# Kernel optimization log

Measured on AMD Instinct MI355X. Metric: run time of the kernel, lower is better.

Reference implementation:

```python
import jax, jax.numpy as jnp
import numpy as np

NUM_HEADS = 14
NUM_KV_HEADS = 2
HEAD_DIM = 64
HIDDEN = 896
ROPE_THETA = 1000000.0
NEG_INF = -1e9


def _rope_tables(seq_len, dtype=jnp.float32):
    inv_freq = 1.0 / (ROPE_THETA ** (jnp.arange(0, HEAD_DIM, 2, dtype=jnp.float32) / HEAD_DIM))
    t = jnp.arange(seq_len, dtype=jnp.float32)
    freqs = t[:, None] * inv_freq[None, :]          # [S, hd/2]
    emb = jnp.concatenate((freqs, freqs), axis=-1)  # [S, hd]
    return jnp.cos(emb).astype(dtype), jnp.sin(emb).astype(dtype)


def _rotate_half(x):
    x1, x2 = x[..., : x.shape[-1] // 2], x[..., x.shape[-1] // 2 :]
    return jnp.concatenate((-x2, x1), axis=-1)


def setup_inputs() -> dict:
    key = jax.random.key(0)
    ks = jax.random.split(key, 6)
    B, S = 2, 2048
    hidden_states = jax.random.normal(ks[0], (B, S, HIDDEN), dtype=jnp.float32)
    # additive causal mask [1, 1, S, S]
    causal = jnp.tril(jnp.ones((S, S), dtype=bool))
    attention_mask = jnp.where(causal, 0.0, NEG_INF).astype(jnp.float32)[None, None]
    sd = 1.0 / np.sqrt(HIDDEN)
    Wq = jax.random.normal(ks[1], (HIDDEN, NUM_HEADS * HEAD_DIM), dtype=jnp.float32) * sd
    bq = jnp.zeros((NUM_HEADS * HEAD_DIM,), dtype=jnp.float32)
    Wk = jax.random.normal(ks[2], (HIDDEN, NUM_KV_HEADS * HEAD_DIM), dtype=jnp.float32) * sd
    bk = jnp.zeros((NUM_KV_HEADS * HEAD_DIM,), dtype=jnp.float32)
    Wv = jax.random.normal(ks[3], (HIDDEN, NUM_KV_HEADS * HEAD_DIM), dtype=jnp.float32) * sd
    bv = jnp.zeros((NUM_KV_HEADS * HEAD_DIM,), dtype=jnp.float32)
    Wo = jax.random.normal(ks[4], (NUM_HEADS * HEAD_DIM, HIDDEN), dtype=jnp.float32) * sd
    return {
        'hidden_states': hidden_states, 'attention_mask': attention_mask,
        'Wq': Wq, 'bq': bq, 'Wk': Wk, 'bk': bk, 'Wv': Wv, 'bv': bv, 'Wo': Wo,
    }


def reference(hidden_states, attention_mask, Wq, bq, Wk, bk, Wv, bv, Wo):
    B, S, _ = hidden_states.shape
    n_groups = NUM_HEADS // NUM_KV_HEADS
    q = (hidden_states @ Wq + bq).reshape(B, S, NUM_HEADS, HEAD_DIM)
    k = (hidden_states @ Wk + bk).reshape(B, S, NUM_KV_HEADS, HEAD_DIM)
    v = (hidden_states @ Wv + bv).reshape(B, S, NUM_KV_HEADS, HEAD_DIM)

    cos, sin = _rope_tables(S, hidden_states.dtype)
    cos = cos[None, :, None, :]
    sin = sin[None, :, None, :]
    q = q * cos + _rotate_half(q) * sin
    k = k * cos + _rotate_half(k) * sin

    # GQA: repeat kv heads to match query heads
    k = jnp.repeat(k, n_groups, axis=2)  # [B, S, nH, hd]
    v = jnp.repeat(v, n_groups, axis=2)

    q = q.transpose(0, 2, 1, 3)  # [B, nH, S, hd]
    k = k.transpose(0, 2, 1, 3)
    v = v.transpose(0, 2, 1, 3)

    scores = jnp.einsum('bhqd,bhkd->bhqk', q, k) / jnp.sqrt(jnp.float32(HEAD_DIM)).astype(q.dtype)
    scores = scores + attention_mask
    attn = jax.nn.softmax(scores, axis=-1)
    out = jnp.einsum('bhqk,bhkd->bhqd', attn, v)        # [B, nH, S, hd]
    out = out.transpose(0, 2, 1, 3).reshape(B, S, -1)   # [B, S, nH*hd]
    return out @ Wo
```

## Files before the change

kernel.cpp:

```cpp
#include <hip/hip_runtime.h>
#include <hip/hip_bf16.h>
#include <math.h>

#define NH 14
#define NKV 2
#define HD 64
#define HID 896
#define SEQ 2048
#define BATCH 2
#define KT 28

typedef __attribute__((ext_vector_type(8))) short short8;
typedef __attribute__((ext_vector_type(4))) float f32x4;
typedef unsigned short ushort_t;

__device__ __forceinline__ unsigned short f2b(float f) {
    unsigned int u = __float_as_uint(f);
    unsigned int r = (u + 0x7fffu + ((u >> 16) & 1u)) >> 16;
    return (unsigned short)r;
}

__device__ __forceinline__ float exp2fast(float x) {
    return __builtin_amdgcn_exp2f(x);
}

__global__ __launch_bounds__(256) void xcast_kernel(
    const float* __restrict__ X, ushort_t* __restrict__ Xb)
{
    size_t i = ((size_t)blockIdx.x * 256 + threadIdx.x) * 8;
    float4 a = *(const float4*)(X + i);
    float4 b = *(const float4*)(X + i + 4);
    short8 o;
    o[0] = f2b(a.x); o[1] = f2b(a.y); o[2] = f2b(a.z); o[3] = f2b(a.w);
    o[4] = f2b(b.x); o[5] = f2b(b.y); o[6] = f2b(b.z); o[7] = f2b(b.w);
    *(short8*)(Xb + i) = o;
}

__global__ __launch_bounds__(256) void wtrans_kernel(
    const float* __restrict__ Wq, const float* __restrict__ Wk,
    const float* __restrict__ Wv, const float* __restrict__ Wo,
    ushort_t* __restrict__ WqkvT, ushort_t* __restrict__ WoT)
{
    __shared__ float tile[32][33];
    const int tx = threadIdx.x, ty = threadIdx.y;
    const int z = blockIdx.z;
    const float* src; ushort_t* dst; int N, rowoff;
    if      (z == 0) { src = Wq; dst = WqkvT; N = HID; rowoff = 0;    }
    else if (z == 1) { src = Wk; dst = WqkvT; N = 128; rowoff = 896;  }
    else if (z == 2) { src = Wv; dst = WqkvT; N = 128; rowoff = 1024; }
    else             { src = Wo; dst = WoT;   N = HID; rowoff = 0;    }
    const int k0 = blockIdx.x * 32;
    const int n0 = blockIdx.y * 32;
    if (n0 >= N) return;
    #pragma unroll
    for (int i = 0; i < 4; ++i)
        tile[ty * 4 + i][tx] = src[(size_t)(k0 + ty * 4 + i) * N + n0 + tx];
    __syncthreads();
    #pragma unroll
    for (int i = 0; i < 4; ++i)
        dst[(size_t)(rowoff + n0 + ty * 4 + i) * HID + k0 + tx]
            = f2b(tile[tx][ty * 4 + i]);
}

#define LDA 40
__global__ __launch_bounds__(256) void qkv_kernel(
    const ushort_t* __restrict__ Xb, const ushort_t* __restrict__ WqkvT,
    const float* __restrict__ bq, const float* __restrict__ bk,
    const float* __restrict__ bv,
    ushort_t* __restrict__ qbuf, ushort_t* __restrict__ kbuf,
    ushort_t* __restrict__ vbuf)
{
    __shared__ ushort_t Asb[2][128 * LDA];
    __shared__ ushort_t Bsb[2][64 * LDA];
    const int tid  = threadIdx.x;
    const int w    = tid >> 6;
    const int lane = tid & 63;
    const int quad = lane >> 4;
    const int l16  = lane & 15;
    const int m0 = blockIdx.x * 128;
    const int nt = blockIdx.y;
    const int nb = nt * 64;

    const int ar0 = tid >> 2;
    const int ac8 = tid & 3;
    const ushort_t* Ag0 = Xb + (size_t)(m0 + ar0) * HID + ac8 * 8;
    const ushort_t* Ag1 = Xb + (size_t)(m0 + ar0 + 64) * HID + ac8 * 8;
    const ushort_t* Bg  = WqkvT + (size_t)(nb + ar0) * HID + ac8 * 8;

    f32x4 acc[2][4];
    #pragma unroll
    for (int mf = 0; mf < 2; ++mf)
        #pragma unroll
        for (int nf = 0; nf < 4; ++nf) acc[mf][nf] = (f32x4){0.f, 0.f, 0.f, 0.f};

    short8 aReg0, aReg1, bReg;
    aReg0 = *(const short8*)(Ag0);
    aReg1 = *(const short8*)(Ag1);
    bReg  = *(const short8*)(Bg);
    *(short8*)&Asb[0][ar0 * LDA + ac8 * 8]        = aReg0;
    *(short8*)&Asb[0][(ar0 + 64) * LDA + ac8 * 8] = aReg1;
    *(short8*)&Bsb[0][ar0 * LDA + ac8 * 8]        = bReg;
    aReg0 = *(const short8*)(Ag0 + 32);
    aReg1 = *(const short8*)(Ag1 + 32);
    bReg  = *(const short8*)(Bg  + 32);

    for (int ks = 0; ks < KT; ++ks) {
        __syncthreads();
        const int cur = ks & 1;
        if (ks + 1 < KT) {
            *(short8*)&Asb[cur ^ 1][ar0 * LDA + ac8 * 8]        = aReg0;
            *(short8*)&Asb[cur ^ 1][(ar0 + 64) * LDA + ac8 * 8] = aReg1;
            *(short8*)&Bsb[cur ^ 1][ar0 * LDA + ac8 * 8]        = bReg;
        }
        if (ks + 2 < KT) {
            aReg0 = *(const short8*)(Ag0 + (ks + 2) * 32);
            aReg1 = *(const short8*)(Ag1 + (ks + 2) * 32);
            bReg  = *(const short8*)(Bg  + (ks + 2) * 32);
        }
        const ushort_t* Ab = &Asb[cur][(w * 32 + l16) * LDA + quad * 8];
        short8 a0 = *(const short8*)Ab;
        short8 a1 = *(const short8*)(Ab + 16 * LDA);
        #pragma unroll
        for (int nf = 0; nf < 4; ++nf) {
            short8 bf = *(const short8*)&Bsb[cur][(nf * 16 + l16) * LDA + quad * 8];
            acc[0][nf] = __builtin_amdgcn_mfma_f32_16x16x32_bf16(a0, bf, acc[0][nf], 0, 0, 0);
            acc[1][nf] = __builtin_amdgcn_mfma_f32_16x16x32_bf16(a1, bf, acc[1][nf], 0, 0, 0);
        }
    }

    float bcol[4];
    #pragma unroll
    for (int f = 0; f < 4; ++f) {
        int d = f * 16 + l16;
        bcol[f] = (nt < 14) ? bq[nt * 64 + d]
                : (nt < 16) ? bk[(nt - 14) * 64 + d]
                            : bv[(nt - 16) * 64 + d];
    }
    const float lnth = 13.815510558f;
    float if0 = expf(-((float)l16)        / 32.0f * lnth);
    float if1 = expf(-((float)(l16 + 16)) / 32.0f * lnth);

    #pragma unroll
    for (int mf = 0; mf < 2; ++mf)
        #pragma unroll
        for (int r = 0; r < 4; ++r) {
            int grow = m0 + w * 32 + mf * 16 + quad * 4 + r;
            int b = grow >> 11;
            int s = grow & 2047;
            float v0 = acc[mf][0][r] + bcol[0];
            float v1 = acc[mf][1][r] + bcol[1];
            float v2 = acc[mf][2][r] + bcol[2];
            float v3 = acc[mf][3][r] + bcol[3];
            if (nt < 16) {
                float s0, c0, s1, c1;
                sincosf((float)s * if0, &s0, &c0);
                sincosf((float)s * if1, &s1, &c1);
                float n0 = v0 * c0 - v2 * s0;
                float n2 = v2 * c0 + v0 * s0;
                float n1 = v1 * c1 - v3 * s1;
                float n3 = v3 * c1 + v1 * s1;
                v0 = n0; v1 = n1; v2 = n2; v3 = n3;
            }
            if (nt < 14) {
                const float qs = 0.18033688f;
                v0 *= qs; v1 *= qs; v2 *= qs; v3 *= qs;
                ushort_t* dst = qbuf + ((size_t)(b * NH + nt) * SEQ + s) * HD;
                dst[l16]      = f2b(v0);
                dst[l16 + 16] = f2b(v1);
                dst[l16 + 32] = f2b(v2);
                dst[l16 + 48] = f2b(v3);
            } else if (nt < 16) {
                ushort_t* dst = kbuf + ((size_t)(b * NKV + nt - 14) * SEQ + s) * HD;
                dst[l16]      = f2b(v0);
                dst[l16 + 16] = f2b(v1);
                dst[l16 + 32] = f2b(v2);
                dst[l16 + 48] = f2b(v3);
            } else {
                ushort_t* dst = vbuf + (size_t)(b * NKV + nt - 16) * HD * SEQ + s;
                dst[(size_t)(l16)      * SEQ] = f2b(v0);
                dst[(size_t)(l16 + 16) * SEQ] = f2b(v1);
                dst[(size_t)(l16 + 32) * SEQ] = f2b(v2);
                dst[(size_t)(l16 + 48) * SEQ] = f2b(v3);
            }
        }
}

#define LDP 76
#define SMMAX 12.0f
__global__ __launch_bounds__(256) void attn_kernel(
    const ushort_t* __restrict__ qbuf, const ushort_t* __restrict__ kbuf,
    const ushort_t* __restrict__ vbuf, ushort_t* __restrict__ abuf)
{
    __shared__ ushort_t Ks[64 * LDP];
    __shared__ ushort_t Vt[64 * LDP];
    __shared__ ushort_t Ps[4][16 * LDP];

    const int tid  = threadIdx.x;
    const int w    = tid >> 6;
    const int lane = tid & 63;
    const int quad = lane >> 4;
    const int l16  = lane & 15;
    const int qt = 31 - blockIdx.x;
    const int h  = blockIdx.y;
    const int b  = blockIdx.z;
    const int kvh = h / (NH / NKV);

    const ushort_t* kb_h = kbuf + (size_t)(b * NKV + kvh) * SEQ * HD;
    const ushort_t* vt_h = vbuf + (size_t)(b * NKV + kvh) * HD * SEQ;

    const int srow = tid >> 3;
    const int sc8  = tid & 7;
    const ushort_t* Kg0 = kb_h + (size_t)srow * HD + sc8 * 8;
    const ushort_t* Kg1 = kb_h + (size_t)(srow + 32) * HD + sc8 * 8;
    const ushort_t* Vg0 = vt_h + (size_t)srow * SEQ + sc8 * 8;
    const ushort_t* Vg1 = vt_h + (size_t)(srow + 32) * SEQ + sc8 * 8;

    const ushort_t* qrow =
        qbuf + ((size_t)((b * NH + h) * SEQ) + qt * 64 + w * 16 + l16) * HD;
    short8 qf0 = *(const short8*)(qrow + quad * 8);
    short8 qf1 = *(const short8*)(qrow + 32 + quad * 8);

    short8 onesb;
    #pragma unroll
    for (int i = 0; i < 8; ++i) onesb[i] = (short)0x3F80;

    f32x4 O[4];
    f32x4 La;
    #pragma unroll
    for (int n = 0; n < 4; ++n) O[n] = (f32x4){0.f, 0.f, 0.f, 0.f};
    La = (f32x4){0.f, 0.f, 0.f, 0.f};

    short8 kr0 = *(const short8*)(Kg0);
    short8 kr1 = *(const short8*)(Kg1);
    short8 vr0 = *(const short8*)(Vg0);
    short8 vr1 = *(const short8*)(Vg1);

    for (int kt = 0; kt <= qt; ++kt) {
        __syncthreads();
        *(short8*)&Ks[srow * LDP + sc8 * 8]        = kr0;
        *(short8*)&Ks[(srow + 32) * LDP + sc8 * 8] = kr1;
        *(short8*)&Vt[srow * LDP + sc8 * 8]        = vr0;
        *(short8*)&Vt[(srow + 32) * LDP + sc8 * 8] = vr1;
        __syncthreads();
        if (kt < qt) {
            kr0 = *(const short8*)(Kg0 + (size_t)(kt + 1) * 64 * HD);
            kr1 = *(const short8*)(Kg1 + (size_t)(kt + 1) * 64 * HD);
            vr0 = *(const short8*)(Vg0 + (kt + 1) * 64);
            vr1 = *(const short8*)(Vg1 + (kt + 1) * 64);
        }

        f32x4 S[4];
        #pragma unroll
        for (int f = 0; f < 4; ++f) {
            short8 kf0 = *(const short8*)&Ks[(f * 16 + l16) * LDP + quad * 8];
            short8 kf1 = *(const short8*)&Ks[(f * 16 + l16) * LDP + 32 + quad * 8];
            S[f] = (f32x4){0.f, 0.f, 0.f, 0.f};
            S[f] = __builtin_amdgcn_mfma_f32_16x16x32_bf16(qf0, kf0, S[f], 0, 0, 0);
            S[f] = __builtin_amdgcn_mfma_f32_16x16x32_bf16(qf1, kf1, S[f], 0, 0, 0);
        }

        if (kt == qt) {
            #pragma unroll
            for (int f = 0; f < 4; ++f)
                #pragma unroll
                for (int r = 0; r < 4; ++r)
                    if ((f * 16 + l16) > (w * 16 + quad * 4 + r))
                        S[f][r] = -1e30f;
        }
        #pragma unroll
        for (int f = 0; f < 4; ++f)
            #pragma unroll
            for (int r = 0; r < 4; ++r)
                Ps[w][(quad * 4 + r) * LDP + f * 16 + l16]
                    = f2b(exp2fast(S[f][r] - SMMAX));

        short8 pa0 = *(const short8*)&Ps[w][l16 * LDP + quad * 8];
        short8 pa1 = *(const short8*)&Ps[w][l16 * LDP + 32 + quad * 8];

        La = __builtin_amdgcn_mfma_f32_16x16x32_bf16(pa0, onesb, La, 0, 0, 0);
        La = __builtin_amdgcn_mfma_f32_16x16x32_bf16(pa1, onesb, La, 0, 0, 0);
        #pragma unroll
        for (int n = 0; n < 4; ++n) {
            short8 vf0 = *(const short8*)&Vt[(n * 16 + l16) * LDP + quad * 8];
            short8 vf1 = *(const short8*)&Vt[(n * 16 + l16) * LDP + 32 + quad * 8];
            O[n] = __builtin_amdgcn_mfma_f32_16x16x32_bf16(pa0, vf0, O[n], 0, 0, 0);
            O[n] = __builtin_amdgcn_mfma_f32_16x16x32_bf16(pa1, vf1, O[n], 0, 0, 0);
        }
    }

    float inv[4];
    #pragma unroll
    for (int r = 0; r < 4; ++r) inv[r] = 1.0f / La[r];
    #pragma unroll
    for (int n = 0; n < 4; ++n)
        #pragma unroll
        for (int r = 0; r < 4; ++r) {
            int rowg = qt * 64 + w * 16 + quad * 4 + r;
            abuf[(size_t)(b * SEQ + rowg) * HID + h * HD + n * 16 + l16]
                = f2b(O[n][r] * inv[r]);
        }
}

__global__ __launch_bounds__(256) void oproj_kernel(
    const ushort_t* __restrict__ A, const ushort_t* __restrict__ WoT,
    float* __restrict__ out)
{
    __shared__ ushort_t Asb[2][128 * LDA];
    __shared__ ushort_t Bsb[2][64 * LDA];
    const int tid  = threadIdx.x;
    const int w    = tid >> 6;
    const int lane = tid & 63;
    const int quad = lane >> 4;
    const int l16  = lane & 15;
    const int m0 = blockIdx.x * 128;
    const int n0 = blockIdx.y * 64;

    const int ar0 = tid >> 2;
    const int ac8 = tid & 3;
    const ushort_t* Ag0 = A + (size_t)(m0 + ar0) * HID + ac8 * 8;
    const ushort_t* Ag1 = A + (size_t)(m0 + ar0 + 64) * HID + ac8 * 8;
    const ushort_t* Bg  = WoT + (size_t)(n0 + ar0) * HID + ac8 * 8;

    f32x4 acc[2][4];
    #pragma unroll
    for (int mf = 0; mf < 2; ++mf)
        #pragma unroll
        for (int nf = 0; nf < 4; ++nf) acc[mf][nf] = (f32x4){0.f, 0.f, 0.f, 0.f};

    short8 aReg0, aReg1, bReg;
    aReg0 = *(const short8*)(Ag0);
    aReg1 = *(const short8*)(Ag1);
    bReg  = *(const short8*)(Bg);
    *(short8*)&Asb[0][ar0 * LDA + ac8 * 8]        = aReg0;
    *(short8*)&Asb[0][(ar0 + 64) * LDA + ac8 * 8] = aReg1;
    *(short8*)&Bsb[0][ar0 * LDA + ac8 * 8]        = bReg;
    aReg0 = *(const short8*)(Ag0 + 32);
    aReg1 = *(const short8*)(Ag1 + 32);
    bReg  = *(const short8*)(Bg  + 32);

    for (int ks = 0; ks < KT; ++ks) {
        __syncthreads();
        const int cur = ks & 1;
        if (ks + 1 < KT) {
            *(short8*)&Asb[cur ^ 1][ar0 * LDA + ac8 * 8]        = aReg0;
            *(short8*)&Asb[cur ^ 1][(ar0 + 64) * LDA + ac8 * 8] = aReg1;
            *(short8*)&Bsb[cur ^ 1][ar0 * LDA + ac8 * 8]        = bReg;
        }
        if (ks + 2 < KT) {
            aReg0 = *(const short8*)(Ag0 + (ks + 2) * 32);
            aReg1 = *(const short8*)(Ag1 + (ks + 2) * 32);
            bReg  = *(const short8*)(Bg  + (ks + 2) * 32);
        }
        const ushort_t* Ab = &Asb[cur][(w * 32 + l16) * LDA + quad * 8];
        short8 a0 = *(const short8*)Ab;
        short8 a1 = *(const short8*)(Ab + 16 * LDA);
        #pragma unroll
        for (int nf = 0; nf < 4; ++nf) {
            short8 bf = *(const short8*)&Bsb[cur][(nf * 16 + l16) * LDA + quad * 8];
            acc[0][nf] = __builtin_amdgcn_mfma_f32_16x16x32_bf16(a0, bf, acc[0][nf], 0, 0, 0);
            acc[1][nf] = __builtin_amdgcn_mfma_f32_16x16x32_bf16(a1, bf, acc[1][nf], 0, 0, 0);
        }
    }

    #pragma unroll
    for (int mf = 0; mf < 2; ++mf)
        #pragma unroll
        for (int r = 0; r < 4; ++r) {
            size_t rbase = (size_t)(m0 + w * 32 + mf * 16 + quad * 4 + r) * HID + n0;
            #pragma unroll
            for (int f = 0; f < 4; ++f)
                out[rbase + f * 16 + l16] = acc[mf][f][r];
        }
}

extern "C" void kernel_launch(void* const* d_in, const int* in_sizes, int n_in,
                              void* d_out, int out_size, void* d_ws, size_t ws_size,
                              hipStream_t stream) {
    const float* X  = (const float*)d_in[0];
    const float* Wq = (const float*)d_in[2];
    const float* bq = (const float*)d_in[3];
    const float* Wk = (const float*)d_in[4];
    const float* bk = (const float*)d_in[5];
    const float* Wv = (const float*)d_in[6];
    const float* bv = (const float*)d_in[7];
    const float* Wo = (const float*)d_in[8];
    float* out = (float*)d_out;

    ushort_t* ws    = (ushort_t*)d_ws;
    ushort_t* Xb    = ws;
    ushort_t* WqkvT = Xb    + 3670016;
    ushort_t* WoT   = WqkvT + 1032192;
    ushort_t* qbuf  = WoT   + 802816;
    ushort_t* kbuf  = qbuf  + 3670016;
    ushort_t* vbuf  = kbuf  + 524288;
    ushort_t* abufb = vbuf  + 524288;

    xcast_kernel<<<dim3(1792), 256, 0, stream>>>(X, Xb);
    wtrans_kernel<<<dim3(28, 28, 4), dim3(32, 8), 0, stream>>>(
        Wq, Wk, Wv, Wo, WqkvT, WoT);
    qkv_kernel<<<dim3(32, 18), 256, 0, stream>>>(
        Xb, WqkvT, bq, bk, bv, qbuf, kbuf, vbuf);
    attn_kernel<<<dim3(32, NH, BATCH), 256, 0, stream>>>(
        qbuf, kbuf, vbuf, abufb);
    oproj_kernel<<<dim3(32, 14), 256, 0, stream>>>(
        abufb, WoT, out);
}
```

Baseline: 199.3 us.

## Process two query tiles per attention block to reuse staged K/V tiles

Each attention block now handles 128 query rows, as two 64-row sub-tiles per wave set, instead of 64. Each K/V tile loaded into shared memory is used by both sub-tiles, which halves the K/V global loads and LDS staging per query row. The causal mask is applied separately on each sub-tile's diagonal, and the first sub-tile skips its last K tile. The grid shrinks to 16 blocks per head with more registers per thread, which lowers parallelism and makes the causal work imbalance across blocks coarser. A launch-bounds occupancy hint is added.

```diff
diff --git a/kernel.cpp b/kernel.cpp
--- a/kernel.cpp
+++ b/kernel.cpp
@@ -187,20 +187,20 @@
 
 #define LDP 76
 #define SMMAX 12.0f
-__global__ __launch_bounds__(256) void attn_kernel(
+__global__ __launch_bounds__(256, 4) void attn_kernel(
     const ushort_t* __restrict__ qbuf, const ushort_t* __restrict__ kbuf,
     const ushort_t* __restrict__ vbuf, ushort_t* __restrict__ abuf)
 {
     __shared__ ushort_t Ks[64 * LDP];
     __shared__ ushort_t Vt[64 * LDP];
-    __shared__ ushort_t Ps[4][16 * LDP];
+    __shared__ ushort_t Ps[4][32 * LDP];
 
     const int tid  = threadIdx.x;
     const int w    = tid >> 6;
     const int lane = tid & 63;
     const int quad = lane >> 4;
     const int l16  = lane & 15;
-    const int qt = 31 - blockIdx.x;
+    const int qt = 15 - blockIdx.x;
     const int h  = blockIdx.y;
     const int b  = blockIdx.z;
     const int kvh = h / (NH / NKV);
@@ -215,89 +215,118 @@
     const ushort_t* Vg0 = vt_h + (size_t)srow * SEQ + sc8 * 8;
     const ushort_t* Vg1 = vt_h + (size_t)(srow + 32) * SEQ + sc8 * 8;
 
-    const ushort_t* qrow =
-        qbuf + ((size_t)((b * NH + h) * SEQ) + qt * 64 + w * 16 + l16) * HD;
-    short8 qf0 = *(const short8*)(qrow + quad * 8);
-    short8 qf1 = *(const short8*)(qrow + 32 + quad * 8);
+    const ushort_t* qbase =
+        qbuf + ((size_t)((b * NH + h) * SEQ) + qt * 128 + w * 16 + l16) * HD;
+    short8 qa0 = *(const short8*)(qbase + quad * 8);
+    short8 qa1 = *(const short8*)(qbase + 32 + quad * 8);
+    short8 qb0 = *(const short8*)(qbase + (size_t)64 * HD + quad * 8);
+    short8 qb1 = *(const short8*)(qbase + (size_t)64 * HD + 32 + quad * 8);
 
     short8 onesb;
     #pragma unroll
     for (int i = 0; i < 8; ++i) onesb[i] = (short)0x3F80;
 
-    f32x4 O[4];
-    f32x4 La;
-    #pragma unroll
-    for (int n = 0; n < 4; ++n) O[n] = (f32x4){0.f, 0.f, 0.f, 0.f};
-    La = (f32x4){0.f, 0.f, 0.f, 0.f};
+    f32x4 O0[4], O1[4], La0, La1;
+    #pragma unroll
+    for (int n = 0; n < 4; ++n) {
+        O0[n] = (f32x4){0.f, 0.f, 0.f, 0.f};
+        O1[n] = (f32x4){0.f, 0.f, 0.f, 0.f};
+    }
+    La0 = (f32x4){0.f, 0.f, 0.f, 0.f};
+    La1 = (f32x4){0.f, 0.f, 0.f, 0.f};
+
+    const int ktmax = 2 * qt + 1;
 
     short8 kr0 = *(const short8*)(Kg0);
     short8 kr1 = *(const short8*)(Kg1);
     short8 vr0 = *(const short8*)(Vg0);
     short8 vr1 = *(const short8*)(Vg1);
 
-    for (int kt = 0; kt <= qt; ++kt) {
+    for (int kt = 0; kt <= ktmax; ++kt) {
         __syncthreads();
         *(short8*)&Ks[srow * LDP + sc8 * 8]        = kr0;
         *(short8*)&Ks[(srow + 32) * LDP + sc8 * 8] = kr1;
         *(short8*)&Vt[srow * LDP + sc8 * 8]        = vr0;
         *(short8*)&Vt[(srow + 32) * LDP + sc8 * 8] = vr1;
         __syncthreads();
-        if (kt < qt) {
+        if (kt < ktmax) {
             kr0 = *(const short8*)(Kg0 + (size_t)(kt + 1) * 64 * HD);
             kr1 = *(const short8*)(Kg1 + (size_t)(kt + 1) * 64 * HD);
             vr0 = *(const short8*)(Vg0 + (kt + 1) * 64);
             vr1 = *(const short8*)(Vg1 + (kt + 1) * 64);
         }
 
-        f32x4 S[4];
+        const bool act0  = (kt <= 2 * qt);
+        const bool diag0 = (kt == 2 * qt);
+        const bool diag1 = (kt == ktmax);
+
         #pragma unroll
         for (int f = 0; f < 4; ++f) {
             short8 kf0 = *(const short8*)&Ks[(f * 16 + l16) * LDP + quad * 8];
             short8 kf1 = *(const short8*)&Ks[(f * 16 + l16) * LDP + 32 + quad * 8];
-            S[f] = (f32x4){0.f, 0.f, 0.f, 0.f};
-            S[f] = __builtin_amdgcn_mfma_f32_16x16x32_bf16(qf0, kf0, S[f], 0, 0, 0);
-            S[f] = __builtin_amdgcn_mfma_f32_16x16x32_bf16(qf1, kf1, S[f], 0, 0, 0);
-        }
-
-        if (kt == qt) {
+            f32x4 s1 = (f32x4){0.f, 0.f, 0.f, 0.f};
+            s1 = __builtin_amdgcn_mfma_f32_16x16x32_bf16(qb0, kf0, s1, 0, 0, 0);
+            s1 = __builtin_amdgcn_mfma_f32_16x16x32_bf16(qb1, kf1, s1, 0, 0, 0);
+            f32x4 s0 = (f32x4){0.f, 0.f, 0.f, 0.f};
+            if (act0) {
+                s0 = __builtin_amdgcn_mfma_f32_16x16x32_bf16(qa0, kf0, s0, 0, 0, 0);
+                s0 = __builtin_amdgcn_mfma_f32_16x16x32_bf16(qa1, kf1, s0, 0, 0, 0);
+            }
             #pragma unroll
-            for (int f = 0; f < 4; ++f)
+            for (int r = 0; r < 4; ++r) {
+                float v1 = s1[r];
+                if (diag1 && (f * 16 + l16) > (w * 16 + quad * 4 + r)) v1 = -1e30f;
+                Ps[w][(16 + quad * 4 + r) * LDP + f * 16 + l16]
+                    = f2b(exp2fast(v1 - SMMAX));
+            }
+            if (act0) {
                 #pragma unroll
-                for (int r = 0; r < 4; ++r)
-                    if ((f * 16 + l16) > (w * 16 + quad * 4 + r))
-                        S[f][r] = -1e30f;
-        }
-        #pragma unroll
-        for (int f = 0; f < 4; ++f)
-            #pragma unroll
-            for (int r = 0; r < 4; ++r)
-                Ps[w][(quad * 4 + r) * LDP + f * 16 + l16]
-                    = f2b(exp2fast(S[f][r] - SMMAX));
-
-        short8 pa0 = *(const short8*)&Ps[w][l16 * LDP + quad * 8];
-        short8 pa1 = *(const short8*)&Ps[w][l16 * LDP + 32 + quad * 8];
-
-        La = __builtin_amdgcn_mfma_f32_16x16x32_bf16(pa0, onesb, La, 0, 0, 0);
-        La = __builtin_amdgcn_mfma_f32_16x16x32_bf16(pa1, onesb, La, 0, 0, 0);
+                for (int r = 0; r < 4; ++r) {
+                    float v0 = s0[r];
+                    if (diag0 && (f * 16 + l16) > (w * 16 + quad * 4 + r)) v0 = -1e30f;
+                    Ps[w][(quad * 4 + r) * LDP + f * 16 + l16]
+                        = f2b(exp2fast(v0 - SMMAX));
+                }
+            }
+        }
+
+        short8 pa1_0 = *(const short8*)&Ps[w][(16 + l16) * LDP + quad * 8];
+        short8 pa1_1 = *(const short8*)&Ps[w][(16 + l16) * LDP + 32 + quad * 8];
+        La1 = __builtin_amdgcn_mfma_f32_16x16x32_bf16(pa1_0, onesb, La1, 0, 0, 0);
+        La1 = __builtin_amdgcn_mfma_f32_16x16x32_bf16(pa1_1, onesb, La1, 0, 0, 0);
+        short8 pa0_0 = pa1_0, pa0_1 = pa1_1;
+        if (act0) {
+            pa0_0 = *(const short8*)&Ps[w][l16 * LDP + quad * 8];
+            pa0_1 = *(const short8*)&Ps[w][l16 * LDP + 32 + quad * 8];
+            La0 = __builtin_amdgcn_mfma_f32_16x16x32_bf16(pa0_0, onesb, La0, 0, 0, 0);
+            La0 = __builtin_amdgcn_mfma_f32_16x16x32_bf16(pa0_1, onesb, La0, 0, 0, 0);
+        }
+
         #pragma unroll
         for (int n = 0; n < 4; ++n) {
             short8 vf0 = *(const short8*)&Vt[(n * 16 + l16) * LDP + quad * 8];
             short8 vf1 = *(const short8*)&Vt[(n * 16 + l16) * LDP + 32 + quad * 8];
-            O[n] = __builtin_amdgcn_mfma_f32_16x16x32_bf16(pa0, vf0, O[n], 0, 0, 0);
-            O[n] = __builtin_amdgcn_mfma_f32_16x16x32_bf16(pa1, vf1, O[n], 0, 0, 0);
+            O1[n] = __builtin_amdgcn_mfma_f32_16x16x32_bf16(pa1_0, vf0, O1[n], 0, 0, 0);
+            O1[n] = __builtin_amdgcn_mfma_f32_16x16x32_bf16(pa1_1, vf1, O1[n], 0, 0, 0);
+            if (act0) {
+                O0[n] = __builtin_amdgcn_mfma_f32_16x16x32_bf16(pa0_0, vf0, O0[n], 0, 0, 0);
+                O0[n] = __builtin_amdgcn_mfma_f32_16x16x32_bf16(pa0_1, vf1, O0[n], 0, 0, 0);
+            }
         }
     }
 
-    float inv[4];
-    #pragma unroll
-    for (int r = 0; r < 4; ++r) inv[r] = 1.0f / La[r];
+    float inv0[4], inv1[4];
+    #pragma unroll
+    for (int r = 0; r < 4; ++r) { inv0[r] = 1.0f / La0[r]; inv1[r] = 1.0f / La1[r]; }
     #pragma unroll
     for (int n = 0; n < 4; ++n)
         #pragma unroll
         for (int r = 0; r < 4; ++r) {
-            int rowg = qt * 64 + w * 16 + quad * 4 + r;
-            abuf[(size_t)(b * SEQ + rowg) * HID + h * HD + n * 16 + l16]
-                = f2b(O[n][r] * inv[r]);
+            int rowg0 = qt * 128 + w * 16 + quad * 4 + r;
+            abuf[(size_t)(b * SEQ + rowg0) * HID + h * HD + n * 16 + l16]
+                = f2b(O0[n][r] * inv0[r]);
+            abuf[(size_t)(b * SEQ + rowg0 + 64) * HID + h * HD + n * 16 + l16]
+                = f2b(O1[n][r] * inv1[r]);
         }
 }
 
@@ -400,7 +429,7 @@
         Wq, Wk, Wv, Wo, WqkvT, WoT);
     qkv_kernel<<<dim3(32, 18), 256, 0, stream>>>(
         Xb, WqkvT, bq, bk, bv, qbuf, kbuf, vbuf);
-    attn_kernel<<<dim3(32, NH, BATCH), 256, 0, stream>>>(
+    attn_kernel<<<dim3(16, NH, BATCH), 256, 0, stream>>>(
         qbuf, kbuf, vbuf, abufb);
     oproj_kernel<<<dim3(32, 14), 256, 0, stream>>>(
         abufb, WoT, out);
```

Result: faster. 195.3 us (-2.0%).
